# Performance work log

Hardware: AMD Instinct MI355X
Metric: run time of the kernel (lower is better)

The kernel has to match this reference:

```python
import jax, jax.numpy as jnp
import numpy as np

N, IN_DIM, HID, HEADS = 20000, 3000, 128, 4
S_DIM, P_DIM = 32, 32
E = 320000
NEG_SLOPE = 0.2
ETA = 1e-6


def _glorot(key, shape):
    fan_in, fan_out = shape[0], shape[-1] if len(shape) > 1 else shape[0]
    lim = np.sqrt(6.0 / (fan_in + fan_out))
    return jax.random.uniform(key, shape, jnp.float32, -lim, lim)


def _gat_params(key, in_dim, out_ch, heads, concat):
    k1, k2, k3 = jax.random.split(key, 3)
    Wl = _glorot(k1, (in_dim, heads * out_ch))
    Wr = _glorot(k2, (in_dim, heads * out_ch))
    att = _glorot(k3, (heads, out_ch))
    b = jnp.zeros((heads * out_ch,) if concat else (out_ch,), jnp.float32)
    return Wl, Wr, att, b


def setup_inputs() -> dict:
    key = jax.random.key(0)
    ks = jax.random.split(key, 6)
    x = jax.random.normal(ks[0], (N, IN_DIM), jnp.float32)
    edge_index = jax.random.randint(ks[1], (2, E), 0, N, jnp.int32)
    out = {"x": x, "edge_index": edge_index}
    for name, kk, (ind, oc, h, cc) in [
        ("s1", ks[2], (IN_DIM, HID, HEADS, True)),
        ("s2", ks[3], (HID * HEADS, S_DIM * 2, 1, False)),
        ("p1", ks[4], (IN_DIM, HID, HEADS, True)),
        ("p2", ks[5], (HID * HEADS, P_DIM * 2, 1, False)),
    ]:
        Wl, Wr, att, b = _gat_params(kk, ind, oc, h, cc)
        out[f"Wl_{name}"] = Wl
        out[f"Wr_{name}"] = Wr
        out[f"att_{name}"] = att
        out[f"b_{name}"] = b
    return out


def gatv2(x, src, dst, Wl, Wr, att, b, heads, out_ch, concat):
    n = x.shape[0]
    xl = (x @ Wl).reshape(n, heads, out_ch)  # source transform
    xr = (x @ Wr).reshape(n, heads, out_ch)  # target transform
    m = xl[src]                                           # [E, H, C] messages
    e = jnp.sum(att * jax.nn.leaky_relu(m + xr[dst], NEG_SLOPE), axis=-1)  # [E, H]
    emax = jax.ops.segment_max(e, dst, num_segments=n)    # self-loops -> no empty segments
    ee = jnp.exp(e - emax[dst])
    denom = jax.ops.segment_sum(ee, dst, num_segments=n)
    alpha = ee / denom[dst]                               # segment softmax over incoming edges
    agg = jax.ops.segment_sum(m * alpha[..., None], dst, num_segments=n)  # [N, H, C]
    out = agg.reshape(n, heads * out_ch) if concat else agg.mean(axis=1)
    return out + b


def reference(x, edge_index, Wl_s1, Wr_s1, att_s1, b_s1, Wl_s2, Wr_s2, att_s2, b_s2,
              Wl_p1, Wr_p1, att_p1, b_p1, Wl_p2, Wr_p2, att_p2, b_p2):
    n = x.shape[0]
    loop = jnp.arange(n, dtype=edge_index.dtype)
    src = jnp.concatenate([edge_index[0], loop])  # add_self_loops (PyG default)
    dst = jnp.concatenate([edge_index[1], loop])
    s = jax.nn.relu(gatv2(x, src, dst, Wl_s1, Wr_s1, att_s1, b_s1, HEADS, HID, True))
    s = gatv2(s, src, dst, Wl_s2, Wr_s2, att_s2, b_s2, 1, S_DIM * 2, False)
    p = gatv2(x, src, dst, Wl_p1, Wr_p1, att_p1, b_p1, HEADS, HID, True)
    p = gatv2(p, src, dst, Wl_p2, Wr_p2, att_p2, b_p2, 1, P_DIM * 2, False)
    mu = jnp.concatenate([s[:, :S_DIM], p[:, :P_DIM]], axis=-1)
    sig = jnp.concatenate([jax.nn.softplus(s[:, S_DIM:]) + ETA,
                           jax.nn.softplus(p[:, P_DIM:]) + ETA], axis=-1)
    return mu, sig
```

## Files before the change

kernel.cpp:

```cpp
#include <hip/hip_runtime.h>
#include <cstdint>

#define NN     20000
#define NE     320000
#define ETOT   340000
#define K1R    3000
#define K1     3072
#define NPAD   20224
#define NCOL1  2048
#define LDA2   1024
#define MU_SZ  1280000

typedef __bf16 bf16x8 __attribute__((ext_vector_type(8)));
typedef float f32x4 __attribute__((ext_vector_type(4)));
typedef unsigned short u16x8 __attribute__((ext_vector_type(8)));

__device__ inline unsigned short f2bf(float f) {
  union { float f; unsigned u; } v; v.f = f;
  unsigned r = v.u + 0x7FFFu + ((v.u >> 16) & 1u);
  return (unsigned short)(r >> 16);
}
__device__ inline float bf2f(unsigned short h) {
  union { unsigned u; float f; } v; v.u = ((unsigned)h) << 16;
  return v.f;
}

typedef const __attribute__((address_space(1))) void* gas1_t;
typedef __attribute__((address_space(3))) void* las3_t;
__device__ inline void llds16(const void* g, void* l) {
  __builtin_amdgcn_global_load_lds((gas1_t)(uintptr_t)g,
                                   (las3_t)(uint32_t)(uintptr_t)l, 16, 0, 0);
}


__global__ __launch_bounds__(256)
void k_convert_x(const float* __restrict__ X, unsigned short* __restrict__ Xb) {
  const int CH = K1 / 8;
  int idx = blockIdx.x * 256 + threadIdx.x;
  if (idx >= NPAD * CH) return;
  int r = idx / CH, c8 = (idx % CH) * 8;
  u16x8 o;
  if (r < NN && c8 < K1R) {
    const float4* p = (const float4*)(X + (size_t)r * K1R + c8);
    float4 a = p[0], b = p[1];
    o[0]=f2bf(a.x); o[1]=f2bf(a.y); o[2]=f2bf(a.z); o[3]=f2bf(a.w);
    o[4]=f2bf(b.x); o[5]=f2bf(b.y); o[6]=f2bf(b.z); o[7]=f2bf(b.w);
  } else {
#pragma unroll
    for (int j = 0; j < 8; j++) o[j] = 0;
  }
  *(u16x8*)(Xb + (size_t)r * K1 + c8) = o;
}

__global__ __launch_bounds__(256)
void k_pack_w1(const float* __restrict__ W0, const float* __restrict__ W1,
               const float* __restrict__ W2, const float* __restrict__ W3,
               unsigned short* __restrict__ Wp) {
  __shared__ float tile[64][65];
  int k0 = blockIdx.x * 64, n0 = blockIdx.y * 64;
  int m = n0 >> 9, c0 = n0 & 511;
  const float* W = (m == 0) ? W0 : (m == 1) ? W1 : (m == 2) ? W2 : W3;
  int tx = threadIdx.x & 63, ty = threadIdx.x >> 6;
#pragma unroll
  for (int rep = 0; rep < 16; rep++) {
    int i = ty + rep * 4;
    int k = k0 + i;
    tile[i][tx] = (k < K1R) ? W[(size_t)k * 512 + c0 + tx] : 0.f;
  }
  __syncthreads();
#pragma unroll
  for (int rep = 0; rep < 16; rep++) {
    int i = ty + rep * 4;
    Wp[(size_t)(n0 + i) * K1 + k0 + tx] = f2bf(tile[tx][i]);
  }
}

__global__ __launch_bounds__(256)
void k_pack_w2(const float* __restrict__ Wl, const float* __restrict__ Wr,
               unsigned short* __restrict__ B2) {
  int idx = blockIdx.x * 256 + threadIdx.x;
  if (idx >= 128 * 1024) return;
  int n = idx >> 10, k = idx & 1023, kk = k & 511;
  float v = (n < 64) ? Wl[(size_t)kk * 64 + n] : Wr[(size_t)kk * 64 + (n - 64)];
  B2[idx] = f2bf(v);
}


__global__ __launch_bounds__(256)
void k_count(const int* __restrict__ ei, int* __restrict__ counts) {
  int e = blockIdx.x * 256 + threadIdx.x;
  if (e >= ETOT) return;
  int dst = (e < NE) ? ei[NE + e] : (e - NE);
  atomicAdd(&counts[dst], 1);
}

__global__ void k_scan(const int* __restrict__ counts, int* __restrict__ row_ptr) {
  __shared__ int part[1024];
  int t = threadIdx.x;
  int base = t * 20;
  int loc[20];
  int s = 0;
#pragma unroll
  for (int i = 0; i < 20; i++) {
    int idx = base + i;
    loc[i] = s;
    s += (idx < NN) ? counts[idx] : 0;
  }
  part[t] = s;
  __syncthreads();
  for (int off = 1; off < 1024; off <<= 1) {
    int v = (t >= off) ? part[t - off] : 0;
    __syncthreads();
    part[t] += v;
    __syncthreads();
  }
  int pre = (t > 0) ? part[t - 1] : 0;
#pragma unroll
  for (int i = 0; i < 20; i++) {
    int idx = base + i;
    if (idx <= NN) row_ptr[idx] = pre + loc[i];
  }
}

__global__ __launch_bounds__(256)
void k_scatter(const int* __restrict__ ei, const int* __restrict__ row_ptr,
               int* __restrict__ fill, int* __restrict__ csr_src) {
  int e = blockIdx.x * 256 + threadIdx.x;
  if (e >= ETOT) return;
  int s_, d_;
  if (e < NE) { s_ = ei[e]; d_ = ei[NE + e]; } else { s_ = d_ = e - NE; }
  int pos = row_ptr[d_] + atomicAdd(&fill[d_], 1);
  csr_src[pos] = s_;
}


#define NT1 48

#define STAGE_ONE do { \
  if (sctr < 4 * NT1) { \
    int ts_ = sctr >> 2, o_ = sctr & 3, sb_ = ts_ & 1; \
    const unsigned short* gb_; char* lb_; int rb_; \
    if (o_ == 0)      { gb_ = A; rb_ = bmBase;       lb_ = lds + (sb_*2+0)*16384; } \
    else if (o_ == 1) { gb_ = B; rb_ = bnBase;       lb_ = lds + 65536 + (sb_*2+0)*16384; } \
    else if (o_ == 2) { gb_ = B; rb_ = bnBase + 128; lb_ = lds + 65536 + (sb_*2+1)*16384; } \
    else              { gb_ = A; rb_ = bmBase + 128; lb_ = lds + (sb_*2+1)*16384; } \
    const unsigned short* g0_ = gb_ + (size_t)(rb_ + trow) * 3072 + ts_ * 64 + scol; \
    llds16(g0_, lb_ + wid * 1024); \
    llds16(g0_ + (size_t)64 * 3072, lb_ + 8192 + wid * 1024); \
    sctr++; \
  } \
} while (0)

#define RDA(DST, BASE) do { \
  _Pragma("unroll") \
  for (int mi = 0; mi < 2; mi++) { \
    int r_ = rw * 32 + mi * 16 + l15; \
    DST[0][mi] = *(const bf16x8*)((BASE) + r_ * 128 + sw0); \
    DST[1][mi] = *(const bf16x8*)((BASE) + r_ * 128 + sw1); \
  } \
} while (0)

#define RDB(DST, BASE) do { \
  _Pragma("unroll") \
  for (int ni = 0; ni < 4; ni++) { \
    int r_ = cw * 64 + ni * 16 + l15; \
    DST[0][ni] = *(const bf16x8*)((BASE) + r_ * 128 + sw0); \
    DST[1][ni] = *(const bf16x8*)((BASE) + r_ * 128 + sw1); \
  } \
} while (0)

#define MF(MH, NH, AV, BV) do { \
  _Pragma("unroll") \
  for (int mi = 0; mi < 2; mi++) \
    _Pragma("unroll") \
    for (int ni = 0; ni < 4; ni++) { \
      acc[MH][NH][mi][ni] = __builtin_amdgcn_mfma_f32_16x16x32_bf16(AV[0][mi], BV[0][ni], acc[MH][NH][mi][ni], 0, 0, 0); \
      acc[MH][NH][mi][ni] = __builtin_amdgcn_mfma_f32_16x16x32_bf16(AV[1][mi], BV[1][ni], acc[MH][NH][mi][ni], 0, 0, 0); \
    } \
} while (0)

#define PH_ENTER do { \
  asm volatile("" ::: "memory"); \
  __builtin_amdgcn_s_barrier(); \
  asm volatile("s_waitcnt lgkmcnt(0)" ::: "memory"); \
  __builtin_amdgcn_sched_barrier(0); \
  __builtin_amdgcn_s_setprio(1); \
} while (0)

#define PH_EXIT do { \
  __builtin_amdgcn_s_setprio(0); \
  __builtin_amdgcn_sched_barrier(0); \
} while (0)

__global__ __launch_bounds__(512, 2)
void gemm256(const unsigned short* __restrict__ A, const unsigned short* __restrict__ B,
             unsigned short* __restrict__ C) {
  __shared__ char lds[131072];
  int tid = threadIdx.x, wid = tid >> 6, lane = tid & 63;
  int l15 = lane & 15;
  int rw = wid & 3, cw = wid >> 2;
  int bid = blockIdx.x;
  int swz = (bid & 7) * 79 + (bid >> 3);
  int bm = swz % 79, bn = swz / 79;
  int bmBase = bm * 256, bnBase = bn * 256;
  int trow = tid >> 3;
  int scol = ((tid & 7) ^ ((tid >> 3) & 7)) * 8;
  int sw0 = (((lane >> 4) + 0) ^ (lane & 7)) * 16;
  int sw1 = (((lane >> 4) + 4) ^ (lane & 7)) * 16;
  f32x4 acc[2][2][2][4] = {};

  int sctr = 0;
  for (int i = 0; i < 4; i++) STAGE_ONE;
  asm volatile("s_waitcnt vmcnt(0)" ::: "memory");
  __builtin_amdgcn_s_barrier();
  asm volatile("" ::: "memory");

  for (int t = 0; t < NT1; t++) {
    int buf = t & 1;
    const char* A0h = lds + (buf * 2 + 0) * 16384;
    const char* A1h = lds + (buf * 2 + 1) * 16384;
    const char* B0h = lds + 65536 + (buf * 2 + 0) * 16384;
    const char* B1h = lds + 65536 + (buf * 2 + 1) * 16384;
    bf16x8 a0[2][2], a1[2][2], b0[2][4], b1[2][4];

    RDA(a0, A0h);
    RDB(b0, B0h);
    STAGE_ONE; STAGE_ONE;
    asm volatile("s_waitcnt vmcnt(4)" ::: "memory");
    PH_ENTER;
    MF(0, 0, a0, b0);
    PH_EXIT;

    RDA(a1, A1h);
    STAGE_ONE; STAGE_ONE;
    PH_ENTER;
    MF(1, 0, a1, b0);
    PH_EXIT;

    RDB(b1, B1h);
    PH_ENTER;
    MF(1, 1, a1, b1);
    PH_EXIT;

    __builtin_amdgcn_s_setprio(1);
    MF(0, 1, a0, b1);
    __builtin_amdgcn_s_setprio(0);
    __builtin_amdgcn_sched_barrier(0);
    asm volatile("s_waitcnt vmcnt(2)" ::: "memory");
    __builtin_amdgcn_s_barrier();
    asm volatile("" ::: "memory");
  }

  unsigned short (*sq)[128] = (unsigned short (*)[128])lds;
#pragma unroll
  for (int mh = 0; mh < 2; mh++)
#pragma unroll
    for (int nh = 0; nh < 2; nh++) {
      __syncthreads();
#pragma unroll
      for (int mi = 0; mi < 2; mi++)
#pragma unroll
        for (int ni = 0; ni < 4; ni++)
#pragma unroll
          for (int r = 0; r < 4; r++)
            sq[rw * 32 + mi * 16 + (lane >> 4) * 4 + r][cw * 64 + ni * 16 + l15] =
                f2bf(acc[mh][nh][mi][ni][r]);
      __syncthreads();
#pragma unroll
      for (int it = 0; it < 4; it++) {
        int idx = it * 512 + tid;
        int row = idx >> 4, ch = idx & 15;
        *(u16x8*)(C + (size_t)(bmBase + mh * 128 + row) * NCOL1 + bnBase + nh * 128 + ch * 8) =
            *(const u16x8*)&sq[row][ch * 8];
      }
    }
}


__global__ __launch_bounds__(256)
void gemm_l2(const unsigned short* __restrict__ As, const unsigned short* __restrict__ Bs,
             float* __restrict__ Cs,
             const unsigned short* __restrict__ Ap, const unsigned short* __restrict__ Bp,
             float* __restrict__ Cp) {
  const int K = LDA2, lda = LDA2, ldb = LDA2, ldc = 128, mreal = NN;
  const unsigned short* A = blockIdx.y ? Ap : As;
  const unsigned short* B = blockIdx.y ? Bp : Bs;
  float* C = blockIdx.y ? Cp : Cs;
  __shared__ char smem_raw[16384];
  unsigned short* sA = (unsigned short*)smem_raw;
  unsigned short* sB = sA + 128 * 32;
  int bm = blockIdx.x;
  int tid = threadIdx.x, wid = tid >> 6, lane = tid & 63;
  int wr = wid >> 1, wc = wid & 1;
  f32x4 acc[4][4] = {};

  int ar = 32 * wid + (lane >> 2);
  int acol = (lane & 3) * 8;
  const unsigned short* Ag = A + (size_t)(bm * 128 + ar) * lda + acol;
  const unsigned short* Bg = B + (size_t)ar * ldb + acol;
  unsigned short* la0 = sA + (wid * 2) * 512;
  unsigned short* lb0 = sB + (wid * 2) * 512;
  int frow = lane & 15, koff = (lane >> 4) * 8;

  for (int kt = 0; kt < K; kt += 32) {
    llds16(Ag + kt, la0);
    llds16(Ag + kt + (size_t)16 * lda, la0 + 512);
    llds16(Bg + kt, lb0);
    llds16(Bg + kt + (size_t)16 * ldb, lb0 + 512);
    __syncthreads();
    bf16x8 af[4], bfr[4];
#pragma unroll
    for (int mi = 0; mi < 4; mi++)
      af[mi] = *(const bf16x8*)(sA + (wr * 64 + mi * 16 + frow) * 32 + koff);
#pragma unroll
    for (int ni = 0; ni < 4; ni++)
      bfr[ni] = *(const bf16x8*)(sB + (wc * 64 + ni * 16 + frow) * 32 + koff);
#pragma unroll
    for (int mi = 0; mi < 4; mi++)
#pragma unroll
      for (int ni = 0; ni < 4; ni++)
        acc[mi][ni] = __builtin_amdgcn_mfma_f32_16x16x32_bf16(af[mi], bfr[ni], acc[mi][ni], 0, 0, 0);
    __syncthreads();
  }

#pragma unroll
  for (int mi = 0; mi < 4; mi++) {
    int grow0 = bm * 128 + wr * 64 + mi * 16 + (lane >> 4) * 4;
#pragma unroll
    for (int ni = 0; ni < 4; ni++) {
      int gcol = wc * 64 + ni * 16 + (lane & 15);
#pragma unroll
      for (int r = 0; r < 4; r++) {
        int grow = grow0 + r;
        if (grow < mreal) C[(size_t)grow * ldc + gcol] = acc[mi][ni][r];
      }
    }
  }
}


__global__ __launch_bounds__(256)
void edge_agg1(const unsigned short* __restrict__ XL1,
               const int* __restrict__ row_ptr, const int* __restrict__ csr_src,
               const float* __restrict__ att_s, const float* __restrict__ att_p,
               const float* __restrict__ b_s, const float* __restrict__ b_p,
               unsigned short* __restrict__ A2s, unsigned short* __restrict__ A2p) {
  int gw = (blockIdx.x * 256 + threadIdx.x) >> 6;
  if (gw >= NN * 2) return;
  int n = gw >> 1, br = gw & 1;
  int lane = threadIdx.x & 63;
  int cb = lane * 8;
  const float* att = br ? att_p : att_s;
  const float* bias = br ? b_p : b_s;
  float xr[8], at[8], agg[8];
  bf16x8 xrv = *(const bf16x8*)(XL1 + (size_t)n * NCOL1 + br * 1024 + 512 + cb);
#pragma unroll
  for (int j = 0; j < 8; j++) { xr[j] = (float)xrv[j]; at[j] = att[cb + j]; agg[j] = 0.f; }
  float M = -1e30f, S = 0.f;
  const size_t srcoff = (size_t)br * 1024 + cb;
  int pe = row_ptr[n + 1];
  for (int p = row_ptr[n]; p < pe; ++p) {
    int src = csr_src[p];
    bf16x8 mv = *(const bf16x8*)(XL1 + (size_t)src * NCOL1 + srcoff);
    float mj[8], part = 0.f;
#pragma unroll
    for (int j = 0; j < 8; j++) {
      mj[j] = (float)mv[j];
      float t = mj[j] + xr[j];
      t = (t > 0.f) ? t : 0.2f * t;
      part = fmaf(at[j], t, part);
    }
#pragma unroll
    for (int w = 1; w < 16; w <<= 1) part += __shfl_xor(part, w);
    float nm = fmaxf(M, part);
    float fac = __expf(M - nm);
    float wgt = __expf(part - nm);
    S = S * fac + wgt;
#pragma unroll
    for (int j = 0; j < 8; j++) agg[j] = agg[j] * fac + wgt * mj[j];
    M = nm;
  }
  float inv = 1.f / S;
  u16x8 hv, lv;
  unsigned short* A2 = br ? A2p : A2s;
#pragma unroll
  for (int j = 0; j < 8; j++) {
    float v = agg[j] * inv + bias[cb + j];
    if (!br) v = fmaxf(v, 0.f);
    unsigned short h = f2bf(v);
    float lo = v - bf2f(h);
    hv[j] = h; lv[j] = f2bf(lo);
  }
  *(u16x8*)(A2 + (size_t)n * LDA2 + cb) = hv;
  *(u16x8*)(A2 + (size_t)n * LDA2 + 512 + cb) = lv;
}


__global__ __launch_bounds__(256)
void edge_agg2(const float* __restrict__ C2s, const float* __restrict__ C2p,
               const int* __restrict__ row_ptr, const int* __restrict__ csr_src,
               const float* __restrict__ att_s, const float* __restrict__ att_p,
               const float* __restrict__ b_s, const float* __restrict__ b_p,
               float* __restrict__ out) {
  int gw = (blockIdx.x * 256 + threadIdx.x) >> 6;
  if (gw >= NN * 2) return;
  int n = gw >> 1, br = gw & 1;
  int lane = threadIdx.x & 63;
  const float* C2 = br ? C2p : C2s;
  float xr = C2[(size_t)n * 128 + 64 + lane];
  float at = (br ? att_p : att_s)[lane];
  float M = -1e30f, S = 0.f, agg = 0.f;
  int pe = row_ptr[n + 1];
  for (int p = row_ptr[n]; p < pe; ++p) {
    int src = csr_src[p];
    float m = C2[(size_t)src * 128 + lane];
    float t = m + xr;
    t = (t > 0.f) ? t : 0.2f * t;
    float part = at * t;
#pragma unroll
    for (int w = 1; w < 64; w <<= 1) part += __shfl_xor(part, w);
    float nm = fmaxf(M, part);
    float fac = __expf(M - nm);
    float wgt = __expf(part - nm);
    S = S * fac + wgt;
    agg = agg * fac + wgt * m;
    M = nm;
  }
  float v = agg / S + (br ? b_p : b_s)[lane];
  if (lane < 32) {
    out[(size_t)n * 64 + br * 32 + lane] = v;
  } else {
    float sp = fmaxf(v, 0.f) + log1pf(__expf(-fabsf(v))) + 1e-6f;
    out[(size_t)MU_SZ + n * 64 + br * 32 + (lane - 32)] = sp;
  }
}


extern "C" void kernel_launch(void* const* d_in, const int* in_sizes, int n_in,
                              void* d_out, int out_size, void* d_ws, size_t ws_size,
                              hipStream_t stream) {
  const float* x      = (const float*)d_in[0];
  const int*   ei     = (const int*)d_in[1];
  const float* Wl_s1  = (const float*)d_in[2];
  const float* Wr_s1  = (const float*)d_in[3];
  const float* att_s1 = (const float*)d_in[4];
  const float* b_s1   = (const float*)d_in[5];
  const float* Wl_s2  = (const float*)d_in[6];
  const float* Wr_s2  = (const float*)d_in[7];
  const float* att_s2 = (const float*)d_in[8];
  const float* b_s2   = (const float*)d_in[9];
  const float* Wl_p1  = (const float*)d_in[10];
  const float* Wr_p1  = (const float*)d_in[11];
  const float* att_p1 = (const float*)d_in[12];
  const float* b_p1   = (const float*)d_in[13];
  const float* Wl_p2  = (const float*)d_in[14];
  const float* Wr_p2  = (const float*)d_in[15];
  const float* att_p2 = (const float*)d_in[16];
  const float* b_p2   = (const float*)d_in[17];

  char* ws = (char*)d_ws;
  unsigned short* Xb   = (unsigned short*)(ws + 0);
  unsigned short* A2s  = (unsigned short*)(ws + 0);
  unsigned short* A2p  = (unsigned short*)(ws + 41156608);
  float*          C2s  = (float*)(ws + 82313216);
  float*          C2p  = (float*)(ws + 92553216);
  unsigned short* B2s  = (unsigned short*)(ws + 102793216);
  unsigned short* B2p  = (unsigned short*)(ws + 103055360);
  unsigned short* Wp   = (unsigned short*)(ws + 124256256);
  unsigned short* XL1  = (unsigned short*)(ws + 136839168);
  int* counts  = (int*)(ws + 219676672);
  int* fill    = (int*)(ws + 219756672);
  int* row_ptr = (int*)(ws + 219836672);
  int* csr_src = (int*)(ws + 219916688);

  hipMemsetAsync(counts, 0, NN * sizeof(int), stream);
  hipMemsetAsync(fill, 0, NN * sizeof(int), stream);

  k_convert_x<<<30336, 256, 0, stream>>>(x, Xb);
  k_pack_w1<<<dim3(48, 32), 256, 0, stream>>>(Wl_s1, Wr_s1, Wl_p1, Wr_p1, Wp);
  k_count<<<(ETOT + 255) / 256, 256, 0, stream>>>(ei, counts);
  k_scan<<<1, 1024, 0, stream>>>(counts, row_ptr);
  k_scatter<<<(ETOT + 255) / 256, 256, 0, stream>>>(ei, row_ptr, fill, csr_src);

  gemm256<<<632, 512, 0, stream>>>(Xb, Wp, XL1);

  k_pack_w2<<<512, 256, 0, stream>>>(Wl_s2, Wr_s2, B2s);
  k_pack_w2<<<512, 256, 0, stream>>>(Wl_p2, Wr_p2, B2p);

  edge_agg1<<<10000, 256, 0, stream>>>(XL1, row_ptr, csr_src, att_s1, att_p1, b_s1, b_p1, A2s, A2p);

  gemm_l2<<<dim3(157, 2), 256, 0, stream>>>(A2s, B2s, C2s, A2p, B2p, C2p);

  edge_agg2<<<10000, 256, 0, stream>>>(C2s, C2p, row_ptr, csr_src, att_s2, att_p2, b_s2, b_p2, (float*)d_out);
}
```

Baseline: 638.1 us.

## Reassign GEMM wave tiles to quadrant layout with per-phase barriers

Changes the layer-1 bf16 GEMM's per-wave work split. Each wave now owns one A half and one B quarter (a 128x64 sub-tile computed as four quadrant phases), instead of 32-row by 64-column slices spread across both halves. Each MFMA phase is now bracketed by workgroup barriers, and the end-of-iteration wait now drains all outstanding global loads (vmcnt(0)). The intent is cleaner LDS read reuse within each phase, at the cost of more synchronisation and less load/compute overlap. It also merges the two layer-2 weight-pack launches into one and simplifies block index computation to an equivalent mapping.

```diff
diff --git a/kernel.cpp b/kernel.cpp
--- a/kernel.cpp
+++ b/kernel.cpp
@@ -76,10 +76,14 @@
 }
 
 __global__ __launch_bounds__(256)
-void k_pack_w2(const float* __restrict__ Wl, const float* __restrict__ Wr,
-               unsigned short* __restrict__ B2) {
-  int idx = blockIdx.x * 256 + threadIdx.x;
-  if (idx >= 128 * 1024) return;
+void k_pack_w2b(const float* __restrict__ Wl_s, const float* __restrict__ Wr_s,
+                const float* __restrict__ Wl_p, const float* __restrict__ Wr_p,
+                unsigned short* __restrict__ B2s, unsigned short* __restrict__ B2p) {
+  int gidx = blockIdx.x * 256 + threadIdx.x;
+  int br = gidx >> 17, idx = gidx & 131071;
+  const float* Wl = br ? Wl_p : Wl_s;
+  const float* Wr = br ? Wr_p : Wr_s;
+  unsigned short* B2 = br ? B2p : B2s;
   int n = idx >> 10, k = idx & 1023, kk = k & 511;
   float v = (n < 64) ? Wl[(size_t)kk * 64 + n] : Wr[(size_t)kk * 64 + (n - 64)];
   B2[idx] = f2bf(v);
@@ -138,11 +142,11 @@
 
 #define STAGE_ONE do { \
   if (sctr < 4 * NT1) { \
-    int ts_ = sctr >> 2, o_ = sctr & 3, sb_ = ts_ & 1; \
+    int ts_ = sctr >> 2, u_ = sctr & 3, sb_ = ts_ & 1; \
     const unsigned short* gb_; char* lb_; int rb_; \
-    if (o_ == 0)      { gb_ = A; rb_ = bmBase;       lb_ = lds + (sb_*2+0)*16384; } \
-    else if (o_ == 1) { gb_ = B; rb_ = bnBase;       lb_ = lds + 65536 + (sb_*2+0)*16384; } \
-    else if (o_ == 2) { gb_ = B; rb_ = bnBase + 128; lb_ = lds + 65536 + (sb_*2+1)*16384; } \
+    if (u_ == 0)      { gb_ = A; rb_ = bmBase;       lb_ = lds + (sb_*2+0)*16384; } \
+    else if (u_ == 1) { gb_ = B; rb_ = bnBase;       lb_ = lds + 65536 + (sb_*2+0)*16384; } \
+    else if (u_ == 2) { gb_ = B; rb_ = bnBase + 128; lb_ = lds + 65536 + (sb_*2+1)*16384; } \
     else              { gb_ = A; rb_ = bmBase + 128; lb_ = lds + (sb_*2+1)*16384; } \
     const unsigned short* g0_ = gb_ + (size_t)(rb_ + trow) * 3072 + ts_ * 64 + scol; \
     llds16(g0_, lb_ + wid * 1024); \
@@ -151,35 +155,35 @@
   } \
 } while (0)
 
-#define RDA(DST, BASE) do { \
+#define RDA_Q(QM, DST) do { \
   _Pragma("unroll") \
-  for (int mi = 0; mi < 2; mi++) { \
-    int r_ = rw * 32 + mi * 16 + l15; \
-    DST[0][mi] = *(const bf16x8*)((BASE) + r_ * 128 + sw0); \
-    DST[1][mi] = *(const bf16x8*)((BASE) + r_ * 128 + sw1); \
+  for (int rt = 0; rt < 4; rt++) { \
+    int r_ = (QM) * 64 + rt * 16 + l15; \
+    DST[0][rt] = *(const bf16x8*)(Ah + r_ * 128 + sw0); \
+    DST[1][rt] = *(const bf16x8*)(Ah + r_ * 128 + sw1); \
   } \
 } while (0)
 
-#define RDB(DST, BASE) do { \
+#define RDB_Q(QN, DST) do { \
   _Pragma("unroll") \
-  for (int ni = 0; ni < 4; ni++) { \
-    int r_ = cw * 64 + ni * 16 + l15; \
-    DST[0][ni] = *(const bf16x8*)((BASE) + r_ * 128 + sw0); \
-    DST[1][ni] = *(const bf16x8*)((BASE) + r_ * 128 + sw1); \
+  for (int ct = 0; ct < 2; ct++) { \
+    int r_ = bcol0 + (QN) * 32 + ct * 16 + l15; \
+    DST[0][ct] = *(const bf16x8*)(Bh + r_ * 128 + sw0); \
+    DST[1][ct] = *(const bf16x8*)(Bh + r_ * 128 + sw1); \
   } \
 } while (0)
 
-#define MF(MH, NH, AV, BV) do { \
+#define MF_Q(QM, QN, AV, BV) do { \
   _Pragma("unroll") \
-  for (int mi = 0; mi < 2; mi++) \
+  for (int rt = 0; rt < 4; rt++) \
     _Pragma("unroll") \
-    for (int ni = 0; ni < 4; ni++) { \
-      acc[MH][NH][mi][ni] = __builtin_amdgcn_mfma_f32_16x16x32_bf16(AV[0][mi], BV[0][ni], acc[MH][NH][mi][ni], 0, 0, 0); \
-      acc[MH][NH][mi][ni] = __builtin_amdgcn_mfma_f32_16x16x32_bf16(AV[1][mi], BV[1][ni], acc[MH][NH][mi][ni], 0, 0, 0); \
+    for (int ct = 0; ct < 2; ct++) { \
+      acc[QM][QN][rt][ct] = __builtin_amdgcn_mfma_f32_16x16x32_bf16(AV[0][rt], BV[0][ct], acc[QM][QN][rt][ct], 0, 0, 0); \
+      acc[QM][QN][rt][ct] = __builtin_amdgcn_mfma_f32_16x16x32_bf16(AV[1][rt], BV[1][ct], acc[QM][QN][rt][ct], 0, 0, 0); \
     } \
 } while (0)
 
-#define PH_ENTER do { \
+#define PH_SYNC do { \
   asm volatile("" ::: "memory"); \
   __builtin_amdgcn_s_barrier(); \
   asm volatile("s_waitcnt lgkmcnt(0)" ::: "memory"); \
@@ -187,9 +191,11 @@
   __builtin_amdgcn_s_setprio(1); \
 } while (0)
 
-#define PH_EXIT do { \
+#define PH_END do { \
   __builtin_amdgcn_s_setprio(0); \
   __builtin_amdgcn_sched_barrier(0); \
+  __builtin_amdgcn_s_barrier(); \
+  asm volatile("" ::: "memory"); \
 } while (0)
 
 __global__ __launch_bounds__(512, 2)
@@ -198,16 +204,16 @@
   __shared__ char lds[131072];
   int tid = threadIdx.x, wid = tid >> 6, lane = tid & 63;
   int l15 = lane & 15;
-  int rw = wid & 3, cw = wid >> 2;
+  int wm = wid >> 2, wn = wid & 3;
+  int bcol0 = (wn & 1) * 64;
   int bid = blockIdx.x;
-  int swz = (bid & 7) * 79 + (bid >> 3);
-  int bm = swz % 79, bn = swz / 79;
+  int bn = bid & 7, bm = bid >> 3;
   int bmBase = bm * 256, bnBase = bn * 256;
   int trow = tid >> 3;
   int scol = ((tid & 7) ^ ((tid >> 3) & 7)) * 8;
   int sw0 = (((lane >> 4) + 0) ^ (lane & 7)) * 16;
   int sw1 = (((lane >> 4) + 4) ^ (lane & 7)) * 16;
-  f32x4 acc[2][2][2][4] = {};
+  f32x4 acc[2][2][4][2] = {};
 
   int sctr = 0;
   for (int i = 0; i < 4; i++) STAGE_ONE;
@@ -217,36 +223,32 @@
 
   for (int t = 0; t < NT1; t++) {
     int buf = t & 1;
-    const char* A0h = lds + (buf * 2 + 0) * 16384;
-    const char* A1h = lds + (buf * 2 + 1) * 16384;
-    const char* B0h = lds + 65536 + (buf * 2 + 0) * 16384;
-    const char* B1h = lds + 65536 + (buf * 2 + 1) * 16384;
-    bf16x8 a0[2][2], a1[2][2], b0[2][4], b1[2][4];
-
-    RDA(a0, A0h);
-    RDB(b0, B0h);
+    const char* Ah = lds + (buf * 2 + wm) * 16384;
+    const char* Bh = lds + 65536 + (buf * 2 + (wn >> 1)) * 16384;
+    bf16x8 a[2][4], b0[2][2], b1[2][2];
+
+    RDA_Q(0, a); RDB_Q(0, b0);
     STAGE_ONE; STAGE_ONE;
-    asm volatile("s_waitcnt vmcnt(4)" ::: "memory");
-    PH_ENTER;
-    MF(0, 0, a0, b0);
-    PH_EXIT;
-
-    RDA(a1, A1h);
+    PH_SYNC;
+    MF_Q(0, 0, a, b0);
+    PH_END;
+
+    RDB_Q(1, b1);
     STAGE_ONE; STAGE_ONE;
-    PH_ENTER;
-    MF(1, 0, a1, b0);
-    PH_EXIT;
-
-    RDB(b1, B1h);
-    PH_ENTER;
-    MF(1, 1, a1, b1);
-    PH_EXIT;
-
-    __builtin_amdgcn_s_setprio(1);
-    MF(0, 1, a0, b1);
+    PH_SYNC;
+    MF_Q(0, 1, a, b1);
+    PH_END;
+
+    RDA_Q(1, a);
+    PH_SYNC;
+    MF_Q(1, 0, a, b0);
+    PH_END;
+
+    PH_SYNC;
+    MF_Q(1, 1, a, b1);
     __builtin_amdgcn_s_setprio(0);
     __builtin_amdgcn_sched_barrier(0);
-    asm volatile("s_waitcnt vmcnt(2)" ::: "memory");
+    asm volatile("s_waitcnt vmcnt(0)" ::: "memory");
     __builtin_amdgcn_s_barrier();
     asm volatile("" ::: "memory");
   }
@@ -257,14 +259,21 @@
 #pragma unroll
     for (int nh = 0; nh < 2; nh++) {
       __syncthreads();
-#pragma unroll
-      for (int mi = 0; mi < 2; mi++)
-#pragma unroll
-        for (int ni = 0; ni < 4; ni++)
-#pragma unroll
-          for (int r = 0; r < 4; r++)
-            sq[rw * 32 + mi * 16 + (lane >> 4) * 4 + r][cw * 64 + ni * 16 + l15] =
-                f2bf(acc[mh][nh][mi][ni][r]);
+      if (wm == mh && (wn >> 1) == nh) {
+#pragma unroll
+        for (int qm = 0; qm < 2; qm++)
+#pragma unroll
+          for (int qn = 0; qn < 2; qn++)
+#pragma unroll
+            for (int rt = 0; rt < 4; rt++)
+#pragma unroll
+              for (int ct = 0; ct < 2; ct++)
+#pragma unroll
+                for (int r = 0; r < 4; r++)
+                  sq[qm * 64 + rt * 16 + (lane >> 4) * 4 + r]
+                    [(wn & 1) * 64 + qn * 32 + ct * 16 + l15] =
+                      f2bf(acc[qm][qn][rt][ct][r]);
+      }
       __syncthreads();
 #pragma unroll
       for (int it = 0; it < 4; it++) {
@@ -484,8 +493,7 @@
 
   gemm256<<<632, 512, 0, stream>>>(Xb, Wp, XL1);
 
-  k_pack_w2<<<512, 256, 0, stream>>>(Wl_s2, Wr_s2, B2s);
-  k_pack_w2<<<512, 256, 0, stream>>>(Wl_p2, Wr_p2, B2p);
+  k_pack_w2b<<<1024, 256, 0, stream>>>(Wl_s2, Wr_s2, Wl_p2, Wr_p2, B2s, B2p);
 
   edge_agg1<<<10000, 256, 0, stream>>>(XL1, row_ptr, csr_src, att_s1, att_p1, b_s1, b_p1, A2s, A2p);
 
```

After: 651.7 us. +2.1%, slower.
